# Kernel tuning notes

Hardware: AMD Instinct MI355X
Metric: run time of the kernel (lower is better)

The kernel has to match this reference:

```python
import jax, jax.numpy as jnp
import numpy as np

EPS = 1e-5
SLOPE = 0.01  # InPlaceABNSync default: leaky_relu(0.01)
SIZES = (1, 2, 3, 6)


def adaptive_avg_pool(x, oh, ow):
    # Matches torch floor/ceil window rule via integral image (single fused op).
    N, C, H, W = x.shape
    S = jnp.pad(x, ((0, 0), (0, 0), (1, 0), (1, 0))).cumsum(2).cumsum(3)
    hs = np.floor(np.arange(oh) * H / oh).astype(np.int32)
    he = np.ceil((np.arange(oh) + 1) * H / oh).astype(np.int32)
    ws = np.floor(np.arange(ow) * W / ow).astype(np.int32)
    we = np.ceil((np.arange(ow) + 1) * W / ow).astype(np.int32)
    sums = (S[:, :, he][:, :, :, we] - S[:, :, hs][:, :, :, we]
            - S[:, :, he][:, :, :, ws] + S[:, :, hs][:, :, :, ws])
    area = ((he - hs)[:, None] * (we - ws)[None, :]).astype(x.dtype)
    return sums / area


def bn_lrelu(x, gamma, beta):
    # BatchNorm (training-mode batch stats, biased var) + leaky_relu, per InPlaceABNSync.
    mean = x.mean((0, 2, 3), keepdims=True)
    var = x.var((0, 2, 3), keepdims=True)
    y = (x - mean) * jax.lax.rsqrt(var + EPS) * gamma[None, :, None, None] + beta[None, :, None, None]
    return jnp.where(y >= 0, y, SLOPE * y)


def upsample_bilinear_ac(x, H, W):
    # align_corners=True bilinear, separable along H then W
    N, C, h, w = x.shape
    yc = jnp.arange(H, dtype=x.dtype) * ((h - 1) / (H - 1) if H > 1 else 0.0)
    xc = jnp.arange(W, dtype=x.dtype) * ((w - 1) / (W - 1) if W > 1 else 0.0)
    y0 = jnp.floor(yc).astype(jnp.int32); y1 = jnp.minimum(y0 + 1, h - 1)
    x0 = jnp.floor(xc).astype(jnp.int32); x1 = jnp.minimum(x0 + 1, w - 1)
    wy = (yc - y0.astype(x.dtype))[None, None, :, None]
    wx = (xc - x0.astype(x.dtype))[None, None, None, :]
    xr = x[:, :, y0, :] * (1 - wy) + x[:, :, y1, :] * wy
    return xr[:, :, :, x0] * (1 - wx) + xr[:, :, :, x1] * wx


def conv1x1(x, w):  # w: [O, I]
    return jnp.einsum('nihw,oi->nohw', x, w)


def conv3x3(x, w):  # w: [O, I, 3, 3]
    return jax.lax.conv_general_dilated(x, w, (1, 1), ((1, 1), (1, 1)),
                                        dimension_numbers=('NCHW', 'OIHW', 'NCHW'))


def setup_inputs() -> dict:
    key = jax.random.key(0)
    ks = jax.random.split(key, 20)
    F_in, F_out = 2048, 512
    inp = {'feats': jax.random.normal(ks[0], (2, F_in, 64, 64), jnp.float32)}
    for s in range(4):
        inp[f'w{s}'] = jax.random.normal(ks[1 + s], (F_out, F_in), jnp.float32) * (F_in ** -0.5)
        inp[f'g{s}'] = jnp.ones((F_out,), jnp.float32)
        inp[f'b{s}'] = jnp.zeros((F_out,), jnp.float32)
    inp['wb'] = jax.random.normal(ks[10], (F_out, F_in + 4 * F_out, 3, 3), jnp.float32) * ((9 * (F_in + 4 * F_out)) ** -0.5)
    inp['gb'] = jnp.ones((F_out,), jnp.float32)
    inp['bb'] = jnp.zeros((F_out,), jnp.float32)
    return inp


def reference(feats, w0, g0, b0, w1, g1, b1, w2, g2, b2, w3, g3, b3, wb, gb, bb):
    H, W = feats.shape[2], feats.shape[3]
    ws = [w0, w1, w2, w3]; gs = [g0, g1, g2, g3]; bs = [b0, b1, b2, b3]
    priors = []
    for s, sz in enumerate(SIZES):
        p = adaptive_avg_pool(feats, sz, sz)
        p = bn_lrelu(conv1x1(p, ws[s]), gs[s], bs[s])
        priors.append(upsample_bilinear_ac(p, H, W))
    priors.append(feats)
    cat = jnp.concatenate(priors, axis=1)
    return bn_lrelu(conv3x3(cat, wb), gb, bb)
```

## Files before the change

kernel.cpp:

```cpp
#include <hip/hip_runtime.h>
#include <stdint.h>


typedef short short8 __attribute__((ext_vector_type(8)));
typedef float f32x4 __attribute__((ext_vector_type(4)));
typedef unsigned short us4 __attribute__((ext_vector_type(4)));

#define PADW   66
#define PLANE  (PADW*PADW)
#define PLANE_ELEMS ((size_t)PLANE*64)

#define POOLED_OFF  0u
#define YS_OFF      819200u
#define STATS_OFF   1024000u
#define CAT_OFF     1048576u
#define CAT_BYTES   71368704u
#define PACKED_OFF  (CAT_OFF + CAT_BYTES)
#define PACKED_BYTES 37748736u
#define CBUF_OFF    (PACKED_OFF + PACKED_BYTES)
#define CBUF_BYTES  16777216u

__device__ __forceinline__ unsigned short f2bf(float x) {
  unsigned int u = __float_as_uint(x);
  unsigned int r = (u + 0x7fffu + ((u >> 16) & 1u)) >> 16;
  return (unsigned short)r;
}

__device__ __forceinline__ void load_lds16(const void* g, uint32_t lds_off) {
  __builtin_amdgcn_global_load_lds(
      (__attribute__((address_space(1))) void*)(uintptr_t)g,
      (__attribute__((address_space(3))) void*)(uintptr_t)lds_off,
      16, 0, 0);
}

__global__ __launch_bounds__(256) void pool_kernel(const float* __restrict__ feats,
                                                   float* __restrict__ pooled) {
  __shared__ float rowtot[64];
  __shared__ float rowseg2[64][2];
  __shared__ float rowseg3[64][3];
  __shared__ float rowseg6[64][6];
  const int t = threadIdx.x;
  const int b = blockIdx.x;
  const float* plane = feats + (size_t)b * 4096;
  const int h = t >> 2, w0 = (t & 3) << 4;
  const int ws3[3] = {0, 21, 42}, we3[3] = {22, 43, 64};
  const int ws6[6] = {0, 10, 21, 32, 42, 53}, we6[6] = {11, 22, 32, 43, 54, 64};
  float p3[3] = {0.f, 0.f, 0.f};
  float p6[6] = {0.f, 0.f, 0.f, 0.f, 0.f, 0.f};
  float tot = 0.f;
  const float4* row = (const float4*)(plane + h * 64 + w0);
#pragma unroll
  for (int i4 = 0; i4 < 4; ++i4) {
    float4 v = row[i4];
    float vals[4] = {v.x, v.y, v.z, v.w};
#pragma unroll
    for (int j = 0; j < 4; ++j) {
      const int w = w0 + i4 * 4 + j;
      const float x = vals[j];
      tot += x;
#pragma unroll
      for (int q = 0; q < 3; ++q) if (w >= ws3[q] && w < we3[q]) p3[q] += x;
#pragma unroll
      for (int q = 0; q < 6; ++q) if (w >= ws6[q] && w < we6[q]) p6[q] += x;
    }
  }
  float pair = tot + __shfl_down(tot, 1, 4);
  float tot4 = pair + __shfl_down(pair, 2, 4);
#pragma unroll
  for (int q = 0; q < 3; ++q) {
    p3[q] += __shfl_down(p3[q], 1, 4);
    p3[q] += __shfl_down(p3[q], 2, 4);
  }
#pragma unroll
  for (int q = 0; q < 6; ++q) {
    p6[q] += __shfl_down(p6[q], 1, 4);
    p6[q] += __shfl_down(p6[q], 2, 4);
  }
  if ((t & 3) == 0) {
    rowtot[h] = tot4;
    rowseg2[h][0] = pair;
#pragma unroll
    for (int q = 0; q < 3; ++q) rowseg3[h][q] = p3[q];
#pragma unroll
    for (int q = 0; q < 6; ++q) rowseg6[h][q] = p6[q];
  }
  if ((t & 3) == 2) rowseg2[h][1] = pair;
  __syncthreads();
  if (t < 50) {
    float s = 0.f;
    float inv;
    if (t == 0) {
      for (int r = 0; r < 64; ++r) s += rowtot[r];
      inv = 1.0f / 4096.0f;
    } else if (t < 5) {
      const int qh = (t - 1) >> 1, qw = (t - 1) & 1;
      for (int r = qh * 32; r < qh * 32 + 32; ++r) s += rowseg2[r][qw];
      inv = 1.0f / 1024.0f;
    } else if (t < 14) {
      const int p = t - 5, qh = p / 3, qw = p % 3;
      for (int r = ws3[qh]; r < we3[qh]; ++r) s += rowseg3[r][qw];
      inv = 1.0f / ((float)(we3[qh] - ws3[qh]) * (float)(we3[qw] - ws3[qw]));
    } else {
      const int p = t - 14, qh = p / 6, qw = p % 6;
      for (int r = ws6[qh]; r < we6[qh]; ++r) s += rowseg6[r][qw];
      inv = 1.0f / ((float)(we6[qh] - ws6[qh]) * (float)(we6[qw] - ws6[qw]));
    }
    const int n = b >> 11, c = b & 2047;
    pooled[((size_t)(n * 50 + t)) * 2048 + c] = s * inv;
  }
}

__global__ __launch_bounds__(256) void conv1x1_kernel(
    const float* __restrict__ pooled, const float* __restrict__ w0,
    const float* __restrict__ w1, const float* __restrict__ w2,
    const float* __restrict__ w3, float* __restrict__ ys) {
  __shared__ float xs[512];
  const int t = threadIdx.x;
  const int col = blockIdx.x >> 2;
  const int kq = blockIdx.x & 3;
  const int n = col / 50, spos = col % 50;
  for (int i = t; i < 512; i += 256)
    xs[i] = pooled[(size_t)col * 2048 + kq * 512 + i];
  __syncthreads();
  int si, pos;
  if (spos < 1)       { si = 0; pos = spos; }
  else if (spos < 5)  { si = 1; pos = spos - 1; }
  else if (spos < 14) { si = 2; pos = spos - 5; }
  else                { si = 3; pos = spos - 14; }
  const float* Wt = (si == 0) ? w0 : (si == 1) ? w1 : (si == 2) ? w2 : w3;
  const int ssarr[4] = {1, 4, 9, 36};
  const int ybase[4] = {0, 1024, 5120, 14336};
  const int ss = ssarr[si];
  for (int o = t; o < 512; o += 256) {
    const float4* wr = (const float4*)(Wt + (size_t)o * 2048 + kq * 512);
    float a = 0.f;
#pragma unroll 4
    for (int c4 = 0; c4 < 128; ++c4) {
      float4 wv = wr[c4];
      a += wv.x * xs[c4 * 4] + wv.y * xs[c4 * 4 + 1] +
           wv.z * xs[c4 * 4 + 2] + wv.w * xs[c4 * 4 + 3];
    }
    atomicAdd(&ys[ybase[si] + (size_t)(n * 512 + o) * ss + pos], a);
  }
}

__global__ __launch_bounds__(512) void bn_small_kernel(
    float* __restrict__ ys, const float* __restrict__ g0, const float* __restrict__ b0,
    const float* __restrict__ g1, const float* __restrict__ b1,
    const float* __restrict__ g2, const float* __restrict__ b2,
    const float* __restrict__ g3, const float* __restrict__ b3) {
  const int si = blockIdx.x;
  const int o = threadIdx.x;
  const int ssarr[4] = {1, 4, 9, 36};
  const int ybase[4] = {0, 1024, 5120, 14336};
  const int ss = ssarr[si];
  const int M = 2 * ss;
  float* base0 = ys + ybase[si] + (size_t)o * ss;
  float* base1 = ys + ybase[si] + (size_t)(512 + o) * ss;
  float sum = 0.f, sq = 0.f;
  for (int p = 0; p < ss; ++p) { float v = base0[p]; sum += v; sq += v * v; }
  for (int p = 0; p < ss; ++p) { float v = base1[p]; sum += v; sq += v * v; }
  const float mean = sum / (float)M;
  float var = sq / (float)M - mean * mean;
  var = fmaxf(var, 0.0f);
  const float rstd = rsqrtf(var + 1e-5f);
  const float* gp = (si == 0) ? g0 : (si == 1) ? g1 : (si == 2) ? g2 : g3;
  const float* bp = (si == 0) ? b0 : (si == 1) ? b1 : (si == 2) ? b2 : b3;
  const float sc = rstd * gp[o];
  const float sh = bp[o] - mean * sc;
  for (int p = 0; p < ss; ++p) {
    float y = base0[p] * sc + sh; base0[p] = (y >= 0.f) ? y : 0.01f * y;
  }
  for (int p = 0; p < ss; ++p) {
    float y = base1[p] * sc + sh; base1[p] = (y >= 0.f) ? y : 0.01f * y;
  }
}

__global__ __launch_bounds__(256) void zero_borders(unsigned short* __restrict__ cat) {
  const int t = threadIdx.x;
  unsigned short* base = cat + (size_t)blockIdx.x * PLANE_ELEMS;
  for (int idx = t; idx < 4160; idx += 256) {
    const int slot = idx >> 4, c4 = idx & 15;
    int q;
    if (slot < 66) q = slot;
    else if (slot < 132) q = 65 * 66 + (slot - 66);
    else { const int k = slot - 132; q = (1 + (k >> 1)) * 66 + (k & 1) * 65; }
    us4 z = {0, 0, 0, 0};
    *(us4*)(base + (size_t)q * 64 + c4 * 4) = z;
  }
}

__global__ __launch_bounds__(256) void fill_priors(const float* __restrict__ ys,
                                                   unsigned short* __restrict__ cat) {
  __shared__ float s0[3072], s1[3072];
  const int t = threadIdx.x;
  const int bx = blockIdx.x;
  const int si = blockIdx.y;
  const int n = bx >> 6, h = bx & 63;
  const int sarr[4] = {1, 2, 3, 6};
  const int ssarr[4] = {1, 4, 9, 36};
  const int ybase[4] = {0, 1024, 5120, 14336};
  const int s = sarr[si], ss = ssarr[si];
  const float yc = (float)(h * (s - 1)) / 63.0f;
  int y0 = (int)yc;
  int y1 = (y0 + 1 < s - 1) ? y0 + 1 : s - 1;
  const float wy = yc - (float)y0;
  const float* base = ys + ybase[si] + (size_t)n * 512 * ss;
  for (int idx = t; idx < 512 * s; idx += 256) {
    int o = idx / s, j = idx - o * s;
    s0[idx] = base[(size_t)o * ss + y0 * s + j];
    s1[idx] = base[(size_t)o * ss + y1 * s + j];
  }
  __syncthreads();
  unsigned short* dstbase = cat + (size_t)(n * 64 + si * 8) * PLANE_ELEMS;
  for (int k = 0; k < 32; ++k) {
    const int g = t + k * 256;
    const int cbp = g >> 10, rem = g & 1023;
    const int w = rem >> 4, c4 = rem & 15;
    const float xc = (float)(w * (s - 1)) / 63.0f;
    int x0 = (int)xc;
    int x1 = (x0 + 1 < s - 1) ? x0 + 1 : s - 1;
    const float wx = xc - (float)x0;
    unsigned short vv[4];
#pragma unroll
    for (int j = 0; j < 4; ++j) {
      const int o = cbp * 64 + c4 * 4 + j;
      const float a = s0[o * s + x0], b2 = s0[o * s + x1];
      const float c = s1[o * s + x0], d = s1[o * s + x1];
      const float top = a + (b2 - a) * wx;
      const float bot = c + (d - c) * wx;
      vv[j] = f2bf(top + (bot - top) * wy);
    }
    us4 ov; ov.x = vv[0]; ov.y = vv[1]; ov.z = vv[2]; ov.w = vv[3];
    const int q = (h + 1) * PADW + (w + 1);
    const int phys = (((c4 >> 1) ^ (q & 7)) << 3) + ((c4 & 1) << 2);
    *(us4*)(dstbase + (size_t)cbp * PLANE_ELEMS + (size_t)q * 64 + phys) = ov;
  }
}

__global__ __launch_bounds__(256) void fill_feats(const float* __restrict__ feats,
                                                  unsigned short* __restrict__ cat) {
  __shared__ float lds[64][65];
  const int t = threadIdx.x;
  const int b = blockIdx.x;
  const int n = b >> 5, fb = b & 31;
  const int h0 = blockIdx.y * 16;
  const float* src = feats + (size_t)(n * 2048 + fb * 64) * 4096;
  unsigned short* dst = cat + (size_t)(n * 64 + 32 + fb) * PLANE_ELEMS;
  for (int h = h0; h < h0 + 16; ++h) {
#pragma unroll
    for (int k = 0; k < 4; ++k) {
      const int idx4 = t + k * 256;
      const int c = idx4 >> 4, w4 = idx4 & 15;
      float4 v = ((const float4*)(src + (size_t)c * 4096 + h * 64))[w4];
      lds[c][w4 * 4 + 0] = v.x; lds[c][w4 * 4 + 1] = v.y;
      lds[c][w4 * 4 + 2] = v.z; lds[c][w4 * 4 + 3] = v.w;
    }
    __syncthreads();
#pragma unroll
    for (int k = 0; k < 4; ++k) {
      const int idx4 = t + k * 256;
      const int w = idx4 >> 4, c4 = idx4 & 15;
      unsigned short vv[4];
#pragma unroll
      for (int j = 0; j < 4; ++j) vv[j] = f2bf(lds[c4 * 4 + j][w]);
      us4 ov; ov.x = vv[0]; ov.y = vv[1]; ov.z = vv[2]; ov.w = vv[3];
      const int q = (h + 1) * PADW + (w + 1);
      const int phys = (((c4 >> 1) ^ (q & 7)) << 3) + ((c4 & 1) << 2);
      *(us4*)(dst + (size_t)q * 64 + phys) = ov;
    }
    __syncthreads();
  }
}

__global__ __launch_bounds__(256) void pack_w(const float* __restrict__ wb,
                                              unsigned short* __restrict__ pk) {
  __shared__ float lds[16][577];
  const int t = threadIdx.x;
  const int cb = blockIdx.x;
  const int ot = blockIdx.y;
  for (int ch8 = 0; ch8 < 8; ++ch8) {
    const int o0 = ot * 128 + ch8 * 16;
    __syncthreads();
#pragma unroll
    for (int k = 0; k < 9; ++k) {
      const int idx4 = t + k * 256;
      const int os = idx4 / 144, c4 = idx4 - os * 144;
      float4 v = ((const float4*)(wb + (size_t)(o0 + os) * 36864 + cb * 576))[c4];
      lds[os][c4 * 4 + 0] = v.x; lds[os][c4 * 4 + 1] = v.y;
      lds[os][c4 * 4 + 2] = v.z; lds[os][c4 * 4 + 3] = v.w;
    }
    __syncthreads();
#pragma unroll
    for (int k = 0; k < 9; ++k) {
      const int g = t + k * 256;
      const int c4 = g & 15;
      const int os = (g >> 4) & 15;
      const int tap = g >> 8;
      unsigned short vv[4];
#pragma unroll
      for (int j = 0; j < 4; ++j) vv[j] = f2bf(lds[os][(c4 * 4 + j) * 9 + tap]);
      us4 ov; ov.x = vv[0]; ov.y = vv[1]; ov.z = vv[2]; ov.w = vv[3];
      const size_t dst = ((size_t)(cb * 9 + tap) * 4 + ot) * 8192 +
                         (size_t)(ch8 * 2 + (c4 >> 3)) * 512 +
                         (size_t)(((c4 >> 1) & 3) * 16 + os) * 8 + (c4 & 1) * 4;
      *(us4*)(pk + dst) = ov;
    }
  }
}

__global__ __launch_bounds__(256, 3) void conv3_kernel(
    const unsigned short* __restrict__ cat, const unsigned short* __restrict__ pk,
    float* __restrict__ C) {
  __shared__ unsigned short As[264 * 64];
  const int t = threadIdx.x;
  const int lane = t & 63;
  const int wave = t >> 6;
  const int lr = lane & 15;
  const int quad = lane >> 4;
  const int bx = blockIdx.x;
  const int by = blockIdx.y;
  const int bz = blockIdx.z;
  const int n = bx >> 5;
  const int h0 = (bx & 31) << 1;
  const int wm = wave >> 1, wn = wave & 1;

  f32x4 acc[4][4];
#pragma unroll
  for (int i = 0; i < 4; ++i)
#pragma unroll
    for (int j = 0; j < 4; ++j) acc[i][j] = (f32x4)0.0f;

  const uint32_t as_base = (uint32_t)(uintptr_t)(&As[0]);
  const uint8_t* catb = (const uint8_t*)cat;
  const unsigned short* pkw = pk + (size_t)by * 8192 + (size_t)(wn * 8) * 512 +
                              (size_t)lane * 8;

  for (int cb2 = 0; cb2 < 16; ++cb2) {
    const int cb = bz * 16 + cb2;
    const uint8_t* srcA = catb +
        ((size_t)(n * 64 + cb) * PLANE_ELEMS + (size_t)(h0 * PADW) * 64) * 2;
    __syncthreads();
    for (int idx = wave; idx < 33; idx += 4)
      load_lds16(srcA + (size_t)idx * 1024 + lane * 16,
                 as_base + (uint32_t)idx * 1024 + lane * 16);
    __syncthreads();
#pragma unroll 3
    for (int tap = 0; tap < 9; ++tap) {
      const int dh = tap / 3 - 1, dw = tap % 3 - 1;
      const int r = wm + 1 + dh;
      const unsigned short* pkt = pkw + (size_t)(cb * 9 + tap) * 32768;
      short8 bf0[4], bf1[4];
#pragma unroll
      for (int j = 0; j < 4; ++j) {
        bf0[j] = *(const short8*)(pkt + (j * 2 + 0) * 512);
        bf1[j] = *(const short8*)(pkt + (j * 2 + 1) * 512);
      }
      short8 af0[4], af1[4];
#pragma unroll
      for (int i = 0; i < 4; ++i) {
        const int s = i * 16 + lr + 1 + dw;
        const int q = (h0 + r) * PADW + s;
        const unsigned short* rowp = As + ((r * 66 + s) << 6);
        af0[i] = *(const short8*)(rowp + ((quad ^ (q & 7)) << 3));
        af1[i] = *(const short8*)(rowp + (((4 + quad) ^ (q & 7)) << 3));
      }
#pragma unroll
      for (int i = 0; i < 4; ++i)
#pragma unroll
        for (int j = 0; j < 4; ++j)
          acc[i][j] = __builtin_amdgcn_mfma_f32_16x16x32_bf16(af0[i], bf0[j],
                                                              acc[i][j], 0, 0, 0);
#pragma unroll
      for (int i = 0; i < 4; ++i)
#pragma unroll
        for (int j = 0; j < 4; ++j)
          acc[i][j] = __builtin_amdgcn_mfma_f32_16x16x32_bf16(af1[i], bf1[j],
                                                              acc[i][j], 0, 0, 0);
    }
  }
  const int row4 = quad * 4;
  const int col = lr;
#pragma unroll
  for (int i = 0; i < 4; ++i) {
    const int m0 = wm * 64 + i * 16 + row4;
#pragma unroll
    for (int j = 0; j < 4; ++j) {
      const int o = by * 128 + wn * 64 + j * 16 + col;
#pragma unroll
      for (int r = 0; r < 4; ++r) {
        const size_t p = (size_t)bx * 128 + m0 + r;
        atomicAdd(&C[p * 512 + o], acc[i][j][r]);
      }
    }
  }
}

__global__ __launch_bounds__(256) void bn_stats_kernel(const float* __restrict__ C,
                                                       float* __restrict__ stats) {
  const int t = threadIdx.x;
  const int p0 = blockIdx.x * 32;
  float s0 = 0.f, q0 = 0.f, s1 = 0.f, q1 = 0.f;
  for (int p = p0; p < p0 + 32; ++p) {
    const float a = C[(size_t)p * 512 + t];
    const float b = C[(size_t)p * 512 + t + 256];
    s0 += a; q0 += a * a; s1 += b; q1 += b * b;
  }
  atomicAdd(&stats[t], s0);
  atomicAdd(&stats[t + 256], s1);
  atomicAdd(&stats[512 + t], q0);
  atomicAdd(&stats[512 + t + 256], q1);
}

__global__ __launch_bounds__(256) void bn_apply_kernel(
    const float* __restrict__ C, const float* __restrict__ stats,
    const float* __restrict__ gb, const float* __restrict__ bb,
    float* __restrict__ out) {
  __shared__ float lds[64][65];
  __shared__ float sc_s[64], sh_s[64];
  const int t = threadIdx.x;
  const int p0 = blockIdx.x * 64;
  const int o0 = blockIdx.y * 64;
  if (t < 64) {
    const int o = o0 + t;
    const float mean = stats[o] * (1.0f / 8192.0f);
    float var = stats[512 + o] * (1.0f / 8192.0f) - mean * mean;
    var = fmaxf(var, 0.0f);
    const float rstd = rsqrtf(var + 1e-5f);
    const float sc = rstd * gb[o];
    sc_s[t] = sc;
    sh_s[t] = bb[o] - mean * sc;
  }
#pragma unroll
  for (int k = 0; k < 4; ++k) {
    const int idx4 = t + k * 256;
    const int ps = idx4 >> 4, o4 = idx4 & 15;
    float4 v = ((const float4*)(C + (size_t)(p0 + ps) * 512 + o0))[o4];
    lds[ps][o4 * 4 + 0] = v.x; lds[ps][o4 * 4 + 1] = v.y;
    lds[ps][o4 * 4 + 2] = v.z; lds[ps][o4 * 4 + 3] = v.w;
  }
  __syncthreads();
  const int n = p0 >> 12, h = (p0 >> 6) & 63;
#pragma unroll
  for (int k = 0; k < 4; ++k) {
    const int idx4 = t + k * 256;
    const int os = idx4 >> 4, w4 = idx4 & 15;
    const float sc = sc_s[os], sh = sh_s[os];
    float vv[4];
#pragma unroll
    for (int j = 0; j < 4; ++j) {
      float v = lds[w4 * 4 + j][os] * sc + sh;
      vv[j] = (v >= 0.f) ? v : 0.01f * v;
    }
    float4 r; r.x = vv[0]; r.y = vv[1]; r.z = vv[2]; r.w = vv[3];
    *(float4*)(out + ((size_t)(n * 512 + o0 + os)) * 4096 + h * 64 + w4 * 4) = r;
  }
}

extern "C" void kernel_launch(void* const* d_in, const int* in_sizes, int n_in,
                              void* d_out, int out_size, void* d_ws, size_t ws_size,
                              hipStream_t stream) {
  (void)in_sizes; (void)n_in; (void)out_size; (void)ws_size;
  const float* feats = (const float*)d_in[0];
  const float* w0 = (const float*)d_in[1];
  const float* g0 = (const float*)d_in[2];
  const float* b0 = (const float*)d_in[3];
  const float* w1 = (const float*)d_in[4];
  const float* g1 = (const float*)d_in[5];
  const float* b1 = (const float*)d_in[6];
  const float* w2 = (const float*)d_in[7];
  const float* g2 = (const float*)d_in[8];
  const float* b2 = (const float*)d_in[9];
  const float* w3 = (const float*)d_in[10];
  const float* g3 = (const float*)d_in[11];
  const float* b3 = (const float*)d_in[12];
  const float* wb = (const float*)d_in[13];
  const float* gb = (const float*)d_in[14];
  const float* bb = (const float*)d_in[15];

  uint8_t* ws = (uint8_t*)d_ws;
  float* pooled = (float*)(ws + POOLED_OFF);
  float* ys = (float*)(ws + YS_OFF);
  float* stats = (float*)(ws + STATS_OFF);
  unsigned short* cat = (unsigned short*)(ws + CAT_OFF);
  unsigned short* pk = (unsigned short*)(ws + PACKED_OFF);
  float* C = (float*)(ws + CBUF_OFF);
  float* outp = (float*)d_out;

  hipMemsetAsync(ys, 0, 204800, stream);
  hipMemsetAsync(stats, 0, 4096, stream);
  hipMemsetAsync(C, 0, CBUF_BYTES, stream);

  pool_kernel<<<4096, 256, 0, stream>>>(feats, pooled);
  conv1x1_kernel<<<400, 256, 0, stream>>>(pooled, w0, w1, w2, w3, ys);
  bn_small_kernel<<<4, 512, 0, stream>>>(ys, g0, b0, g1, b1, g2, b2, g3, b3);
  zero_borders<<<128, 256, 0, stream>>>(cat);
  fill_priors<<<dim3(128, 4), 256, 0, stream>>>(ys, cat);
  fill_feats<<<dim3(64, 4), 256, 0, stream>>>(feats, cat);
  pack_w<<<dim3(64, 4), 256, 0, stream>>>(wb, pk);
  conv3_kernel<<<dim3(64, 4, 4), 256, 0, stream>>>(cat, pk, C);
  bn_stats_kernel<<<256, 256, 0, stream>>>(C, stats);
  bn_apply_kernel<<<dim3(128, 8), 256, 0, stream>>>(C, stats, gb, bb, outp);
}
```

Before: 633.8 us.

## Switch conv3x3 to 32x32x16 MFMA tiles and rework conv1x1 reduction

Measured after the change: 735.0 us. 16.0% more time.

```diff
diff --git a/kernel.cpp b/kernel.cpp
--- a/kernel.cpp
+++ b/kernel.cpp
@@ -4,6 +4,7 @@
 
 typedef short short8 __attribute__((ext_vector_type(8)));
 typedef float f32x4 __attribute__((ext_vector_type(4)));
+typedef float f32x16 __attribute__((ext_vector_type(16)));
 typedef unsigned short us4 __attribute__((ext_vector_type(4)));
 
 #define PADW   66
@@ -114,14 +115,16 @@
     const float* __restrict__ pooled, const float* __restrict__ w0,
     const float* __restrict__ w1, const float* __restrict__ w2,
     const float* __restrict__ w3, float* __restrict__ ys) {
-  __shared__ float xs[512];
-  const int t = threadIdx.x;
+  const int t = threadIdx.x;
+  const int lane = t & 63;
+  const int w = t >> 6;
   const int col = blockIdx.x >> 2;
-  const int kq = blockIdx.x & 3;
+  const int og = blockIdx.x & 3;
   const int n = col / 50, spos = col % 50;
-  for (int i = t; i < 512; i += 256)
-    xs[i] = pooled[(size_t)col * 2048 + kq * 512 + i];
-  __syncthreads();
+  float4 xv[8];
+  const float4* xp = (const float4*)(pooled + (size_t)col * 2048);
+#pragma unroll
+  for (int i = 0; i < 8; ++i) xv[i] = xp[i * 64 + lane];
   int si, pos;
   if (spos < 1)       { si = 0; pos = spos; }
   else if (spos < 5)  { si = 1; pos = spos - 1; }
@@ -131,16 +134,19 @@
   const int ssarr[4] = {1, 4, 9, 36};
   const int ybase[4] = {0, 1024, 5120, 14336};
   const int ss = ssarr[si];
-  for (int o = t; o < 512; o += 256) {
-    const float4* wr = (const float4*)(Wt + (size_t)o * 2048 + kq * 512);
+  for (int oi = 0; oi < 32; ++oi) {
+    const int o = og * 128 + w * 32 + oi;
+    const float4* wr = (const float4*)(Wt + (size_t)o * 2048);
     float a = 0.f;
-#pragma unroll 4
-    for (int c4 = 0; c4 < 128; ++c4) {
-      float4 wv = wr[c4];
-      a += wv.x * xs[c4 * 4] + wv.y * xs[c4 * 4 + 1] +
-           wv.z * xs[c4 * 4 + 2] + wv.w * xs[c4 * 4 + 3];
-    }
-    atomicAdd(&ys[ybase[si] + (size_t)(n * 512 + o) * ss + pos], a);
+#pragma unroll
+    for (int i = 0; i < 8; ++i) {
+      float4 wv = wr[i * 64 + lane];
+      a += wv.x * xv[i].x + wv.y * xv[i].y + wv.z * xv[i].z + wv.w * xv[i].w;
+    }
+#pragma unroll
+    for (int d = 1; d < 64; d <<= 1) a += __shfl_xor(a, d);
+    if (lane == 0)
+      ys[ybase[si] + (size_t)(n * 512 + o) * ss + pos] = a;
   }
 }
 
@@ -301,9 +307,12 @@
 #pragma unroll
       for (int j = 0; j < 4; ++j) vv[j] = f2bf(lds[os][(c4 * 4 + j) * 9 + tap]);
       us4 ov; ov.x = vv[0]; ov.y = vv[1]; ov.z = vv[2]; ov.w = vv[3];
+      const int o_local = ch8 * 16 + os;
+      const int wn = o_local >> 6, jb = (o_local >> 5) & 1, l5 = o_local & 31;
+      const int ks = c4 >> 2, lhi = (c4 >> 1) & 1, e0 = (c4 & 1) * 4;
+      const int f = wn * 8 + jb * 4 + ks;
       const size_t dst = ((size_t)(cb * 9 + tap) * 4 + ot) * 8192 +
-                         (size_t)(ch8 * 2 + (c4 >> 3)) * 512 +
-                         (size_t)(((c4 >> 1) & 3) * 16 + os) * 8 + (c4 & 1) * 4;
+                         (size_t)f * 512 + (size_t)(lhi * 32 + l5) * 8 + e0;
       *(us4*)(pk + dst) = ov;
     }
   }
@@ -316,8 +325,8 @@
   const int t = threadIdx.x;
   const int lane = t & 63;
   const int wave = t >> 6;
-  const int lr = lane & 15;
-  const int quad = lane >> 4;
+  const int l5 = lane & 31;
+  const int lhi = lane >> 5;
   const int bx = blockIdx.x;
   const int by = blockIdx.y;
   const int bz = blockIdx.z;
@@ -325,15 +334,15 @@
   const int h0 = (bx & 31) << 1;
   const int wm = wave >> 1, wn = wave & 1;
 
-  f32x4 acc[4][4];
-#pragma unroll
-  for (int i = 0; i < 4; ++i)
-#pragma unroll
-    for (int j = 0; j < 4; ++j) acc[i][j] = (f32x4)0.0f;
+  f32x16 acc[2][2];
+#pragma unroll
+  for (int i = 0; i < 2; ++i)
+#pragma unroll
+    for (int j = 0; j < 2; ++j) acc[i][j] = (f32x16)0.0f;
 
   const uint32_t as_base = (uint32_t)(uintptr_t)(&As[0]);
   const uint8_t* catb = (const uint8_t*)cat;
-  const unsigned short* pkw = pk + (size_t)by * 8192 + (size_t)(wn * 8) * 512 +
+  const unsigned short* pkw = pk + (size_t)by * 8192 + (size_t)wn * 4096 +
                               (size_t)lane * 8;
 
   for (int cb2 = 0; cb2 < 16; ++cb2) {
@@ -345,52 +354,48 @@
       load_lds16(srcA + (size_t)idx * 1024 + lane * 16,
                  as_base + (uint32_t)idx * 1024 + lane * 16);
     __syncthreads();
-#pragma unroll 3
+#pragma unroll
     for (int tap = 0; tap < 9; ++tap) {
       const int dh = tap / 3 - 1, dw = tap % 3 - 1;
       const int r = wm + 1 + dh;
       const unsigned short* pkt = pkw + (size_t)(cb * 9 + tap) * 32768;
-      short8 bf0[4], bf1[4];
-#pragma unroll
-      for (int j = 0; j < 4; ++j) {
-        bf0[j] = *(const short8*)(pkt + (j * 2 + 0) * 512);
-        bf1[j] = *(const short8*)(pkt + (j * 2 + 1) * 512);
+      short8 bf[2][4];
+#pragma unroll
+      for (int jb = 0; jb < 2; ++jb)
+#pragma unroll
+        for (int ks = 0; ks < 4; ++ks)
+          bf[jb][ks] = *(const short8*)(pkt + (jb * 4 + ks) * 512);
+      short8 af[2][4];
+#pragma unroll
+      for (int im = 0; im < 2; ++im) {
+        const int s = im * 32 + l5 + 1 + dw;
+        const int q = (h0 + r) * PADW + s;
+        const int key = q & 7;
+        const unsigned short* rowp = As + ((r * 66 + s) << 6);
+#pragma unroll
+        for (int ks = 0; ks < 4; ++ks)
+          af[im][ks] = *(const short8*)(rowp + (((ks * 2 + lhi) ^ key) << 3));
       }
-      short8 af0[4], af1[4];
-#pragma unroll
-      for (int i = 0; i < 4; ++i) {
-        const int s = i * 16 + lr + 1 + dw;
-        const int q = (h0 + r) * PADW + s;
-        const unsigned short* rowp = As + ((r * 66 + s) << 6);
-        af0[i] = *(const short8*)(rowp + ((quad ^ (q & 7)) << 3));
-        af1[i] = *(const short8*)(rowp + (((4 + quad) ^ (q & 7)) << 3));
-      }
-#pragma unroll
-      for (int i = 0; i < 4; ++i)
-#pragma unroll
-        for (int j = 0; j < 4; ++j)
-          acc[i][j] = __builtin_amdgcn_mfma_f32_16x16x32_bf16(af0[i], bf0[j],
-                                                              acc[i][j], 0, 0, 0);
-#pragma unroll
-      for (int i = 0; i < 4; ++i)
-#pragma unroll
-        for (int j = 0; j < 4; ++j)
-          acc[i][j] = __builtin_amdgcn_mfma_f32_16x16x32_bf16(af1[i], bf1[j],
-                                                              acc[i][j], 0, 0, 0);
-    }
-  }
-  const int row4 = quad * 4;
-  const int col = lr;
-#pragma unroll
-  for (int i = 0; i < 4; ++i) {
-    const int m0 = wm * 64 + i * 16 + row4;
-#pragma unroll
-    for (int j = 0; j < 4; ++j) {
-      const int o = by * 128 + wn * 64 + j * 16 + col;
-#pragma unroll
-      for (int r = 0; r < 4; ++r) {
-        const size_t p = (size_t)bx * 128 + m0 + r;
-        atomicAdd(&C[p * 512 + o], acc[i][j][r]);
+#pragma unroll
+      for (int ks = 0; ks < 4; ++ks)
+#pragma unroll
+        for (int im = 0; im < 2; ++im)
+#pragma unroll
+          for (int jb = 0; jb < 2; ++jb)
+            acc[im][jb] = __builtin_amdgcn_mfma_f32_32x32x16_bf16(
+                af[im][ks], bf[jb][ks], acc[im][jb], 0, 0, 0);
+    }
+  }
+#pragma unroll
+  for (int im = 0; im < 2; ++im) {
+#pragma unroll
+    for (int jb = 0; jb < 2; ++jb) {
+      const int o = by * 128 + wn * 64 + jb * 32 + l5;
+#pragma unroll
+      for (int r = 0; r < 16; ++r) {
+        const int row = (r & 3) + 8 * (r >> 2) + 4 * lhi;
+        const size_t p = (size_t)bx * 128 + wm * 64 + im * 32 + row;
+        atomicAdd(&C[p * 512 + o], acc[im][jb][r]);
       }
     }
   }
@@ -487,7 +492,6 @@
   float* C = (float*)(ws + CBUF_OFF);
   float* outp = (float*)d_out;
 
-  hipMemsetAsync(ys, 0, 204800, stream);
   hipMemsetAsync(stats, 0, 4096, stream);
   hipMemsetAsync(C, 0, CBUF_BYTES, stream);
 
```

## Prefetch conv3 weight fragments across taps and rework conv1x1 as wave reductions

Applied to the files above, without the earlier changes.

New measurement: 665.9 us. +5.1%, slower.

```diff
diff --git a/kernel.cpp b/kernel.cpp
--- a/kernel.cpp
+++ b/kernel.cpp
@@ -114,14 +114,16 @@
     const float* __restrict__ pooled, const float* __restrict__ w0,
     const float* __restrict__ w1, const float* __restrict__ w2,
     const float* __restrict__ w3, float* __restrict__ ys) {
-  __shared__ float xs[512];
-  const int t = threadIdx.x;
+  const int t = threadIdx.x;
+  const int lane = t & 63;
+  const int w = t >> 6;
   const int col = blockIdx.x >> 2;
-  const int kq = blockIdx.x & 3;
+  const int og = blockIdx.x & 3;
   const int n = col / 50, spos = col % 50;
-  for (int i = t; i < 512; i += 256)
-    xs[i] = pooled[(size_t)col * 2048 + kq * 512 + i];
-  __syncthreads();
+  float4 xv[8];
+  const float4* xp = (const float4*)(pooled + (size_t)col * 2048);
+#pragma unroll
+  for (int i = 0; i < 8; ++i) xv[i] = xp[i * 64 + lane];
   int si, pos;
   if (spos < 1)       { si = 0; pos = spos; }
   else if (spos < 5)  { si = 1; pos = spos - 1; }
@@ -131,16 +133,19 @@
   const int ssarr[4] = {1, 4, 9, 36};
   const int ybase[4] = {0, 1024, 5120, 14336};
   const int ss = ssarr[si];
-  for (int o = t; o < 512; o += 256) {
-    const float4* wr = (const float4*)(Wt + (size_t)o * 2048 + kq * 512);
+  for (int oi = 0; oi < 32; ++oi) {
+    const int o = og * 128 + w * 32 + oi;
+    const float4* wr = (const float4*)(Wt + (size_t)o * 2048);
     float a = 0.f;
-#pragma unroll 4
-    for (int c4 = 0; c4 < 128; ++c4) {
-      float4 wv = wr[c4];
-      a += wv.x * xs[c4 * 4] + wv.y * xs[c4 * 4 + 1] +
-           wv.z * xs[c4 * 4 + 2] + wv.w * xs[c4 * 4 + 3];
-    }
-    atomicAdd(&ys[ybase[si] + (size_t)(n * 512 + o) * ss + pos], a);
+#pragma unroll
+    for (int i = 0; i < 8; ++i) {
+      float4 wv = wr[i * 64 + lane];
+      a += wv.x * xv[i].x + wv.y * xv[i].y + wv.z * xv[i].z + wv.w * xv[i].w;
+    }
+#pragma unroll
+    for (int d = 1; d < 64; d <<= 1) a += __shfl_xor(a, d);
+    if (lane == 0)
+      ys[ybase[si] + (size_t)(n * 512 + o) * ss + pos] = a;
   }
 }
 
@@ -309,7 +314,7 @@
   }
 }
 
-__global__ __launch_bounds__(256, 3) void conv3_kernel(
+__global__ __launch_bounds__(256, 2) void conv3_kernel(
     const unsigned short* __restrict__ cat, const unsigned short* __restrict__ pk,
     float* __restrict__ C) {
   __shared__ unsigned short As[264 * 64];
@@ -336,6 +341,15 @@
   const unsigned short* pkw = pk + (size_t)by * 8192 + (size_t)(wn * 8) * 512 +
                               (size_t)lane * 8;
 
+  int tcb = bz * 144;
+  const int tcb_last = bz * 144 + 143;
+  short8 bfc[8], bfn[8];
+  {
+    const unsigned short* p0 = pkw + (size_t)tcb * 32768;
+#pragma unroll
+    for (int f = 0; f < 8; ++f) bfc[f] = *(const short8*)(p0 + f * 512);
+  }
+
   for (int cb2 = 0; cb2 < 16; ++cb2) {
     const int cb = bz * 16 + cb2;
     const uint8_t* srcA = catb +
@@ -345,38 +359,35 @@
       load_lds16(srcA + (size_t)idx * 1024 + lane * 16,
                  as_base + (uint32_t)idx * 1024 + lane * 16);
     __syncthreads();
-#pragma unroll 3
+#pragma unroll
     for (int tap = 0; tap < 9; ++tap) {
+      const int tnext = (tcb < tcb_last) ? tcb + 1 : tcb_last;
+      const unsigned short* pn = pkw + (size_t)tnext * 32768;
+#pragma unroll
+      for (int f = 0; f < 8; ++f) bfn[f] = *(const short8*)(pn + f * 512);
+
       const int dh = tap / 3 - 1, dw = tap % 3 - 1;
       const int r = wm + 1 + dh;
-      const unsigned short* pkt = pkw + (size_t)(cb * 9 + tap) * 32768;
-      short8 bf0[4], bf1[4];
-#pragma unroll
-      for (int j = 0; j < 4; ++j) {
-        bf0[j] = *(const short8*)(pkt + (j * 2 + 0) * 512);
-        bf1[j] = *(const short8*)(pkt + (j * 2 + 1) * 512);
+#pragma unroll
+      for (int ks = 0; ks < 2; ++ks) {
+        short8 af[4];
+#pragma unroll
+        for (int i = 0; i < 4; ++i) {
+          const int s = i * 16 + lr + 1 + dw;
+          const int q = (h0 + r) * PADW + s;
+          const unsigned short* rowp = As + ((r * 66 + s) << 6);
+          af[i] = *(const short8*)(rowp + (((ks * 4 + quad) ^ (q & 7)) << 3));
+        }
+#pragma unroll
+        for (int i = 0; i < 4; ++i)
+#pragma unroll
+          for (int j = 0; j < 4; ++j)
+            acc[i][j] = __builtin_amdgcn_mfma_f32_16x16x32_bf16(
+                af[i], bfc[j * 2 + ks], acc[i][j], 0, 0, 0);
       }
-      short8 af0[4], af1[4];
-#pragma unroll
-      for (int i = 0; i < 4; ++i) {
-        const int s = i * 16 + lr + 1 + dw;
-        const int q = (h0 + r) * PADW + s;
-        const unsigned short* rowp = As + ((r * 66 + s) << 6);
-        af0[i] = *(const short8*)(rowp + ((quad ^ (q & 7)) << 3));
-        af1[i] = *(const short8*)(rowp + (((4 + quad) ^ (q & 7)) << 3));
-      }
-#pragma unroll
-      for (int i = 0; i < 4; ++i)
-#pragma unroll
-        for (int j = 0; j < 4; ++j)
-          acc[i][j] = __builtin_amdgcn_mfma_f32_16x16x32_bf16(af0[i], bf0[j],
-                                                              acc[i][j], 0, 0, 0);
-#pragma unroll
-      for (int i = 0; i < 4; ++i)
-#pragma unroll
-        for (int j = 0; j < 4; ++j)
-          acc[i][j] = __builtin_amdgcn_mfma_f32_16x16x32_bf16(af1[i], bf1[j],
-                                                              acc[i][j], 0, 0, 0);
+#pragma unroll
+      for (int f = 0; f < 8; ++f) bfc[f] = bfn[f];
+      ++tcb;
     }
   }
   const int row4 = quad * 4;
@@ -487,7 +498,6 @@
   float* C = (float*)(ws + CBUF_OFF);
   float* outp = (float*)d_out;
 
-  hipMemsetAsync(ys, 0, 204800, stream);
   hipMemsetAsync(stats, 0, 4096, stream);
   hipMemsetAsync(C, 0, CBUF_BYTES, stream);
 
```
